# Performance work log

Measured on AMD Instinct MI355X. Metric: run time of the kernel, lower is better.

The kernel has to match this reference:

```python
import jax, jax.numpy as jnp
import numpy as np

XZ = jnp.array([0, 2])
XY = jnp.array([0, 1])
YZ = jnp.array([1, 2])


def _bilinear(plane, uv):
    """plane: (C,R,R) as (C,H,W); uv: (N,2) in [0,1], uv[:,0]->width, uv[:,1]->height.
    Border padding + align_corners=True semantics (grid_sample style)."""
    R = plane.shape[-1]
    xy = jnp.clip(uv, 0.0, 1.0) * (R - 1)
    x, y = xy[:, 0], xy[:, 1]
    x0 = jnp.floor(x)
    y0 = jnp.floor(y)
    x0i = jnp.clip(x0.astype(jnp.int32), 0, R - 1)
    y0i = jnp.clip(y0.astype(jnp.int32), 0, R - 1)
    x1i = jnp.clip(x0i + 1, 0, R - 1)
    y1i = jnp.clip(y0i + 1, 0, R - 1)
    wx = (x - x0)[None, :]  # (1,N)
    wy = (y - y0)[None, :]
    f00 = plane[:, y0i, x0i]  # (C,N)
    f01 = plane[:, y0i, x1i]
    f10 = plane[:, y1i, x0i]
    f11 = plane[:, y1i, x1i]
    top = f00 * (1.0 - wx) + f01 * wx
    bot = f10 * (1.0 - wx) + f11 * wx
    return (top * (1.0 - wy) + bot * wy).T  # (N,C)


def _sample_triplane(p, c_xz, c_xy, c_yz):
    """p: (bs,N,3) in [0,1]; planes: (bs,C,R,R). Returns (bs,N,C) summed over planes."""
    def per_batch(pb, fxz, fxy, fyz):
        return (_bilinear(fxz, pb[:, XZ])
                + _bilinear(fxy, pb[:, XY])
                + _bilinear(fyz, pb[:, YZ]))
    return jax.vmap(per_batch)(p, c_xz, c_xy, c_yz)


def setup_inputs() -> dict:
    key = jax.random.key(0)
    ks = jax.random.split(key, 12)
    bs, ns, C, S, R = 2, 50000, 32, 8, 128
    inp = {
        "query_pos": jax.random.uniform(ks[0], (bs, ns, 3), dtype=jnp.float32),
        "c_xz": jax.random.normal(ks[1], (bs, C, R, R), dtype=jnp.float32),
        "c_xy": jax.random.normal(ks[2], (bs, C, R, R), dtype=jnp.float32),
        "c_yz": jax.random.normal(ks[3], (bs, C, R, R), dtype=jnp.float32),
        # offset weights scaled small so sampled points stay mostly in-bounds
        "W_off": jax.random.normal(ks[4], (C, S * 3), dtype=jnp.float32) * 0.01,
        "b_off": jnp.zeros((S * 3,), dtype=jnp.float32),
        "W_w": jax.random.normal(ks[5], (C, S), dtype=jnp.float32) * 0.1,
        "b_w": jnp.zeros((S,), dtype=jnp.float32),
        "W_v": jax.random.normal(ks[6], (C, C), dtype=jnp.float32) * (1.0 / np.sqrt(C)),
        "b_v": jnp.zeros((C,), dtype=jnp.float32),
        "W_out": jax.random.normal(ks[7], (C, C), dtype=jnp.float32) * (1.0 / np.sqrt(C)),
        "b_out": jnp.zeros((C,), dtype=jnp.float32),
    }
    return inp


def reference(query_pos, c_xz, c_xy, c_yz, W_off, b_off, W_w, b_w, W_v, b_v, W_out, b_out):
    bs, ns, _ = query_pos.shape
    S = W_w.shape[1]
    # round 1: sample tri-plane features at query points
    feature = _sample_triplane(query_pos, c_xz, c_xy, c_yz)  # (bs,ns,C)
    # predict per-query sample offsets and weights
    off = (feature @ W_off + b_off).reshape(bs, ns, S, 3)
    w = (feature @ W_w + b_w).reshape(bs, ns, S, 1)
    pts = off + query_pos[:, :, None, :]  # (bs,ns,S,3)
    # round 2: sample at deformed points
    aux = _sample_triplane(pts.reshape(bs, ns * S, 3), c_xz, c_xy, c_yz)
    v = aux.reshape(bs, ns, S, -1) @ W_v + b_v  # (bs,ns,S,C)
    out = (v * w).sum(-2)                        # weighted reduce over samples
    out = out @ W_out + b_out + feature          # residual
    return out  # (bs,ns,C)
```

## Files before the change

kernel.cpp:

```cpp
#include <hip/hip_runtime.h>
#include <hip/hip_fp16.h>

#define BS 2
#define NS 50000
#define CCH 32
#define RR 128
#define SS 8

typedef float v2f __attribute__((ext_vector_type(2)));
typedef _Float16 h2 __attribute__((ext_vector_type(2)));

#if __has_builtin(__builtin_amdgcn_fdot2)
#define HAVE_DOT2 1
#else
#define HAVE_DOT2 0
#endif


__global__ __launch_bounds__(256)
void prep(const float* __restrict__ cxz,
          const float* __restrict__ cxy,
          const float* __restrict__ cyz,
          const float* __restrict__ Wv, const float* __restrict__ bv,
          const float* __restrict__ Wout,
          unsigned* __restrict__ tp, float* __restrict__ Wc,
          float* __restrict__ bvw) {
    __shared__ float lds[32 * 129];
    int tid = threadIdx.x;
    int row = blockIdx.x;
    if (row < BS * 3 * RR) {
        int y  = row & 127;
        int pl = (row >> 7) % 3;
        int b  = row / 384;
        const float* src = (pl == 0) ? cxz : ((pl == 1) ? cxy : cyz);
        const float* sp = src + (((size_t)(b * CCH)) << 14) + (y << 7);
#pragma unroll
        for (int i = 0; i < 16; ++i) {
            int c = (tid >> 7) + 2 * i;
            int x = tid & 127;
            lds[c * 129 + x] = sp[((size_t)c << 14) + x];
        }
        __syncthreads();
        unsigned* dst = tp + ((size_t)row << 12);
#pragma unroll
        for (int i = 0; i < 16; ++i) {
            int idx = tid + 256 * i;
            int c = idx & 31;
            int x = idx >> 5;
            int x1 = min(x + 1, 127);
            unsigned h0 = __half_as_ushort(__float2half(lds[c * 129 + x]));
            unsigned h1 = __half_as_ushort(__float2half(lds[c * 129 + x1]));
            dst[(x << 5) + c] = h0 | (h1 << 16);
        }
    } else {
        int t = (row - BS * 3 * RR) * 256 + tid;
        int c = t >> 5, j = t & 31;
        float acc = 0.f;
#pragma unroll
        for (int k = 0; k < 32; ++k) acc += Wv[c * 32 + k] * Wout[k * 32 + j];
        Wc[t] = acc;
        if (t < 32) {
            float a2 = 0.f;
#pragma unroll
            for (int k = 0; k < 32; ++k) a2 += bv[k] * Wout[k * 32 + t];
            bvw[t] = a2;
        }
    }
}


struct f4 { v2f lo, hi; };

struct Samp { uint4 u[6]; float wc0, wc1, wr1, wr2; };

__device__ __forceinline__ Samp load_samp(const uint4* __restrict__ P0,
                                          float p0, float p1, float p2) {
    Samp t;
    float x0c = fminf(fmaxf(p0, 0.f), 1.f) * 127.f;
    float x1c = fminf(fmaxf(p1, 0.f), 1.f) * 127.f;
    float x2c = fminf(fmaxf(p2, 0.f), 1.f) * 127.f;
    int i0 = min((int)x0c, 126);
    t.wc0 = x0c - (float)i0;
    int i1 = min((int)x1c, 126);
    t.wc1 = x1c - (float)i1;
    float f1 = floorf(x1c);
    int r10 = (int)f1, r11 = min(r10 + 1, 127);
    t.wr1 = x1c - f1;
    float f2 = floorf(x2c);
    int r20 = (int)f2, r21 = min(r20 + 1, 127);
    t.wr2 = x2c - f2;

    const uint4* Pxz = P0;
    const uint4* Pxy = P0 + (1 << 17);
    const uint4* Pyz = P0 + (2 << 17);
    int c0 = i0 << 3, c1 = i1 << 3;
    int R10 = r10 << 10, R11 = r11 << 10;
    int R20 = r20 << 10, R21 = r21 << 10;
    t.u[0] = Pxz[R20 + c0];  t.u[1] = Pxz[R21 + c0];
    t.u[2] = Pxy[R10 + c0];  t.u[3] = Pxy[R11 + c0];
    t.u[4] = Pyz[R20 + c1];  t.u[5] = Pyz[R21 + c1];
    return t;
}

__device__ __forceinline__ unsigned pack2(float a, float b) {
#if HAVE_DOT2
    return __builtin_bit_cast(unsigned, __builtin_amdgcn_cvt_pkrtz(a, b));
#else
    __half2 h = __floats2half2_rn(a, b);
    return __builtin_bit_cast(unsigned, h);
#endif
}

#if HAVE_DOT2
__device__ __forceinline__ void eval_row(f4& acc, uint4 u, h2 w) {
    acc.lo.x = __builtin_amdgcn_fdot2(__builtin_bit_cast(h2, u.x), w, acc.lo.x, false);
    acc.lo.y = __builtin_amdgcn_fdot2(__builtin_bit_cast(h2, u.y), w, acc.lo.y, false);
    acc.hi.x = __builtin_amdgcn_fdot2(__builtin_bit_cast(h2, u.z), w, acc.hi.x, false);
    acc.hi.y = __builtin_amdgcn_fdot2(__builtin_bit_cast(h2, u.w), w, acc.hi.y, false);
}

__device__ __forceinline__ void eval_plane(f4& acc, uint4 ua, uint4 ub,
                                           float wx, float wy) {
    float wB1 = wx * wy;
    float wB0 = wx - wB1;
    float wA1 = wy - wB1;
    float wA0 = 1.f - wx - wA1;
    h2 w0 = __builtin_bit_cast(h2, __builtin_amdgcn_cvt_pkrtz(wA0, wB0));
    h2 w1 = __builtin_bit_cast(h2, __builtin_amdgcn_cvt_pkrtz(wA1, wB1));
    eval_row(acc, ua, w0);
    eval_row(acc, ub, w1);
}

__device__ __forceinline__ void eval_rowp(f4& acc, uint4 u, unsigned pw) {
    eval_row(acc, u, __builtin_bit_cast(h2, pw));
}
#else
__device__ __forceinline__ void eval_row(f4& acc, uint4 u, float wA, float wB) {
    __half2 h0 = __builtin_bit_cast(__half2, u.x);
    __half2 h1 = __builtin_bit_cast(__half2, u.y);
    __half2 h2_ = __builtin_bit_cast(__half2, u.z);
    __half2 h3 = __builtin_bit_cast(__half2, u.w);
    acc.lo.x = fmaf(__half2float(h0.y), wB, fmaf(__half2float(h0.x), wA, acc.lo.x));
    acc.lo.y = fmaf(__half2float(h1.y), wB, fmaf(__half2float(h1.x), wA, acc.lo.y));
    acc.hi.x = fmaf(__half2float(h2_.y), wB, fmaf(__half2float(h2_.x), wA, acc.hi.x));
    acc.hi.y = fmaf(__half2float(h3.y), wB, fmaf(__half2float(h3.x), wA, acc.hi.y));
}

__device__ __forceinline__ void eval_plane(f4& acc, uint4 ua, uint4 ub,
                                           float wx, float wy) {
    float wB1 = wx * wy;
    float wB0 = wx - wB1;
    float wA1 = wy - wB1;
    float wA0 = 1.f - wx - wA1;
    eval_row(acc, ua, wA0, wB0);
    eval_row(acc, ub, wA1, wB1);
}

__device__ __forceinline__ void eval_rowp(f4& acc, uint4 u, unsigned pw) {
    __half2 hw = __builtin_bit_cast(__half2, pw);
    eval_row(acc, u, __half2float(hw.x), __half2float(hw.y));
}
#endif

__device__ __forceinline__ void eval_samp(const Samp& t, f4& acc) {
    eval_plane(acc, t.u[0], t.u[1], t.wc0, t.wr2);
    eval_plane(acc, t.u[2], t.u[3], t.wc0, t.wr1);
    eval_plane(acc, t.u[4], t.u[5], t.wc1, t.wr2);
}

#define GETE(v, idx) (((idx) & 2) ? (((idx) & 1) ? (v).hi.y : (v).hi.x) \
                                  : (((idx) & 1) ? (v).lo.y : (v).lo.x))
#define GETC(v, idx) __shfl(GETE(v, idx), base | ((idx) >> 2), 64)

struct SampB { uint4 u[6]; };

__global__ __launch_bounds__(256)
void eda_main(const float* __restrict__ qp, const unsigned* __restrict__ tp,
              const float* __restrict__ Woff, const float* __restrict__ boff,
              const float* __restrict__ Ww, const float* __restrict__ bw,
              const float* __restrict__ Wc, const float* __restrict__ bvw,
              const float* __restrict__ bout, float* __restrict__ out) {
    __shared__ float    sWcat[32][32];
    __shared__ unsigned sWc2h[16][32];
    __shared__ float sbcat[32];
    __shared__ float sbvw[32];
    __shared__ float sbout[32];

    int tid = threadIdx.x;
    int lane = tid & 7;
    int base = tid & 56;
    int b  = blockIdx.x & 1;
    int qi = (blockIdx.x >> 1) * 32 + (tid >> 3);
    int qq = min(qi, NS - 1);

    const float* p = qp + ((size_t)b * NS + qq) * 3;
    float p0 = p[0], p1 = p[1], p2 = p[2];

    const uint4* P0 = (const uint4*)tp + (((size_t)(b * 3)) << 17) + lane;

    Samp fs = load_samp(P0, p0, p1, p2);

    for (int i = tid; i < 1024; i += 256) {
        int k = i >> 5, j = i & 31, l2 = j >> 2, e = j & 3;
        sWcat[k][j] = (e < 3) ? Woff[k * 24 + 3 * l2 + e] : Ww[k * 8 + l2];
    }
    {
        int k2 = tid >> 5, j = tid & 31;
        sWc2h[k2][j]     = pack2(Wc[k2 * 64 + j],        Wc[k2 * 64 + 32 + j]);
        sWc2h[k2 + 8][j] = pack2(Wc[(k2 + 8) * 64 + j],  Wc[(k2 + 8) * 64 + 32 + j]);
    }
    if (tid < 32) {
        int l2 = tid >> 2, e = tid & 3;
        sbcat[tid] = (e < 3) ? boff[3 * l2 + e] : bw[l2];
        sbvw[tid]  = bvw[tid];
        sbout[tid] = bout[tid];
    }
    __syncthreads();

    f4 feat; feat.lo = (v2f){0.f, 0.f}; feat.hi = (v2f){0.f, 0.f};
    eval_samp(fs, feat);

    f4 cat;
    cat.lo.x = sbcat[(lane << 2) + 0]; cat.lo.y = sbcat[(lane << 2) + 1];
    cat.hi.x = sbcat[(lane << 2) + 2]; cat.hi.y = sbcat[(lane << 2) + 3];
#pragma unroll
    for (int k = 0; k < 32; ++k) {
        float fc = GETC(feat, k);
        const v2f* wp = (const v2f*)&sWcat[k][lane << 2];
        v2f fc2 = {fc, fc};
        cat.lo = __builtin_elementwise_fma(fc2, wp[0], cat.lo);
        cat.hi = __builtin_elementwise_fma(fc2, wp[1], cat.hi);
    }

    float sx = p0 + cat.lo.x, sy = p1 + cat.lo.y, sz = p2 + cat.hi.x;
    float wt_my = cat.hi.y;
    float x0c = fminf(fmaxf(sx, 0.f), 1.f) * 127.f;
    int  i0 = min((int)x0c, 126);
    float wc0 = x0c - (float)i0;
    float x1c = fminf(fmaxf(sy, 0.f), 1.f) * 127.f;
    int  i1 = min((int)x1c, 126);
    float wc1 = x1c - (float)i1;
    float f1 = floorf(x1c);
    int r10 = (int)f1, r11 = min(r10 + 1, 127);
    float wr1 = x1c - f1;
    float x2c = fminf(fmaxf(sz, 0.f), 1.f) * 127.f;
    float f2 = floorf(x2c);
    int r20 = (int)f2, r21 = min(r20 + 1, 127);
    float wr2 = x2c - f2;
    int c0 = i0 << 3, c1 = i1 << 3;
    int o0 = (r20 << 10) + c0;
    int o1 = (r21 << 10) + c0;
    int o2 = (1 << 17) + (r10 << 10) + c0;
    int o3 = (1 << 17) + (r11 << 10) + c0;
    int o4 = (2 << 17) + (r20 << 10) + c1;
    int o5 = (2 << 17) + (r21 << 10) + c1;
    unsigned m0, m1, m2, m3, m4, m5;
    { float wB1 = wc0 * wr2, wB0 = wc0 - wB1, wA1 = wr2 - wB1, wA0 = 1.f - wc0 - wA1;
      m0 = pack2(wA0, wB0); m1 = pack2(wA1, wB1); }
    { float wB1 = wc0 * wr1, wB0 = wc0 - wB1, wA1 = wr1 - wB1, wA0 = 1.f - wc0 - wA1;
      m2 = pack2(wA0, wB0); m3 = pack2(wA1, wB1); }
    { float wB1 = wc1 * wr2, wB0 = wc1 - wB1, wA1 = wr2 - wB1, wA0 = 1.f - wc1 - wA1;
      m4 = pack2(wA0, wB0); m5 = pack2(wA1, wB1); }

    f4 wa; wa.lo = (v2f){0.f, 0.f}; wa.hi = (v2f){0.f, 0.f};
    float wsum = 0.f;
    SampB cur, nxt;
    {
        int src = base;
        cur.u[0] = P0[__shfl(o0, src, 64)];
        cur.u[1] = P0[__shfl(o1, src, 64)];
        cur.u[2] = P0[__shfl(o2, src, 64)];
        cur.u[3] = P0[__shfl(o3, src, 64)];
        cur.u[4] = P0[__shfl(o4, src, 64)];
        cur.u[5] = P0[__shfl(o5, src, 64)];
    }
#pragma unroll
    for (int s = 0; s < SS; ++s) {
        if (s < SS - 1) {
            int src = base | (s + 1);
            nxt.u[0] = P0[__shfl(o0, src, 64)];
            nxt.u[1] = P0[__shfl(o1, src, 64)];
            nxt.u[2] = P0[__shfl(o2, src, 64)];
            nxt.u[3] = P0[__shfl(o3, src, 64)];
            nxt.u[4] = P0[__shfl(o4, src, 64)];
            nxt.u[5] = P0[__shfl(o5, src, 64)];
        }
        int src = base | s;
        f4 aux; aux.lo = (v2f){0.f, 0.f}; aux.hi = (v2f){0.f, 0.f};
        eval_rowp(aux, cur.u[0], (unsigned)__shfl((int)m0, src, 64));
        eval_rowp(aux, cur.u[1], (unsigned)__shfl((int)m1, src, 64));
        eval_rowp(aux, cur.u[2], (unsigned)__shfl((int)m2, src, 64));
        eval_rowp(aux, cur.u[3], (unsigned)__shfl((int)m3, src, 64));
        eval_rowp(aux, cur.u[4], (unsigned)__shfl((int)m4, src, 64));
        eval_rowp(aux, cur.u[5], (unsigned)__shfl((int)m5, src, 64));
        float wt = __shfl(wt_my, src, 64);
        v2f w2 = {wt, wt};
        wa.lo = __builtin_elementwise_fma(w2, aux.lo, wa.lo);
        wa.hi = __builtin_elementwise_fma(w2, aux.hi, wa.hi);
        wsum += wt;
        if (s < SS - 1) cur = nxt;
    }

    f4 o;
    v2f ws2 = {wsum, wsum};
    {
        v2f bo  = {sbout[(lane << 2) + 0], sbout[(lane << 2) + 1]};
        v2f bv2 = {sbvw[(lane << 2) + 0], sbvw[(lane << 2) + 1]};
        o.lo = __builtin_elementwise_fma(ws2, bv2, bo) + feat.lo;
        v2f bo2 = {sbout[(lane << 2) + 2], sbout[(lane << 2) + 3]};
        v2f bv3 = {sbvw[(lane << 2) + 2], sbvw[(lane << 2) + 3]};
        o.hi = __builtin_elementwise_fma(ws2, bv3, bo2) + feat.hi;
    }
    unsigned pkLo = pack2(wa.lo.x, wa.lo.y);
    unsigned pkHi = pack2(wa.hi.x, wa.hi.y);
#pragma unroll
    for (int k2 = 0; k2 < 16; ++k2) {
        unsigned wb = (unsigned)__shfl((int)((k2 & 1) ? pkHi : pkLo), base | (k2 >> 1), 64);
        const uint4 wv = *(const uint4*)&sWc2h[k2][lane << 2];
#if HAVE_DOT2
        h2 wp = __builtin_bit_cast(h2, wb);
        o.lo.x = __builtin_amdgcn_fdot2(__builtin_bit_cast(h2, wv.x), wp, o.lo.x, false);
        o.lo.y = __builtin_amdgcn_fdot2(__builtin_bit_cast(h2, wv.y), wp, o.lo.y, false);
        o.hi.x = __builtin_amdgcn_fdot2(__builtin_bit_cast(h2, wv.z), wp, o.hi.x, false);
        o.hi.y = __builtin_amdgcn_fdot2(__builtin_bit_cast(h2, wv.w), wp, o.hi.y, false);
#else
        __half2 hw = __builtin_bit_cast(__half2, wb);
        float a0 = __half2float(hw.x), a1 = __half2float(hw.y);
        __half2 w0 = __builtin_bit_cast(__half2, wv.x);
        __half2 w1 = __builtin_bit_cast(__half2, wv.y);
        __half2 w2_ = __builtin_bit_cast(__half2, wv.z);
        __half2 w3 = __builtin_bit_cast(__half2, wv.w);
        o.lo.x = fmaf(__half2float(w0.y), a1, fmaf(__half2float(w0.x), a0, o.lo.x));
        o.lo.y = fmaf(__half2float(w1.y), a1, fmaf(__half2float(w1.x), a0, o.lo.y));
        o.hi.x = fmaf(__half2float(w2_.y), a1, fmaf(__half2float(w2_.x), a0, o.hi.x));
        o.hi.y = fmaf(__half2float(w3.y), a1, fmaf(__half2float(w3.x), a0, o.hi.y));
#endif
    }

    if (qi < NS) {
        float* dst = out + ((size_t)b * NS + qi) * 32 + (lane << 2);
        *(float4*)dst = make_float4(o.lo.x, o.lo.y, o.hi.x, o.hi.y);
    }
}

extern "C" void kernel_launch(void* const* d_in, const int* in_sizes, int n_in,
                              void* d_out, int out_size, void* d_ws, size_t ws_size,
                              hipStream_t stream) {
    const float* qp   = (const float*)d_in[0];
    const float* cxz  = (const float*)d_in[1];
    const float* cxy  = (const float*)d_in[2];
    const float* cyz  = (const float*)d_in[3];
    const float* Woff = (const float*)d_in[4];
    const float* boff = (const float*)d_in[5];
    const float* Ww   = (const float*)d_in[6];
    const float* bw   = (const float*)d_in[7];
    const float* Wv   = (const float*)d_in[8];
    const float* bv   = (const float*)d_in[9];
    const float* Wout = (const float*)d_in[10];
    const float* bout = (const float*)d_in[11];
    float* out = (float*)d_out;

    unsigned* tp = (unsigned*)d_ws;
    float* Wc  = (float*)((char*)d_ws + (size_t)BS * 3 * RR * RR * CCH * 4);
    float* bvw = Wc + 1024;

    prep<<<BS * 3 * RR + 4, 256, 0, stream>>>(cxz, cxy, cyz, Wv, bv, Wout, tp, Wc, bvw);
    int blocks_per_batch = (NS + 31) / 32;
    eda_main<<<2 * blocks_per_batch, 256, 0, stream>>>(qp, tp, Woff, boff, Ww, bw,
                                                       Wc, bvw, bout, out);
}
```

Measured before the change: 129.4 us.

## Store triplane as plain fp16 texels instead of x-pair packed layout

The prep kernel now writes each plane texel once as fp16, with channels contiguous and vectorized float4 reads and uint4 writes. Before, each texel was stored next to its x+1 neighbour in a packed pair. This halves the workspace and the prep write traffic. In exchange the main kernel issues twice as many gathers (two uint2 loads per corner row instead of one uint4) and drops the fdot2 path for scalar half-to-float FMAs. Interpolation weights are also shuffled as packed half fractions, which lowers their precision.

```diff
diff --git a/kernel.cpp b/kernel.cpp
--- a/kernel.cpp
+++ b/kernel.cpp
@@ -16,6 +16,12 @@
 #define HAVE_DOT2 0
 #endif
 
+
+__device__ __forceinline__ unsigned pk_rn(float a, float b) {
+    unsigned h0 = __half_as_ushort(__float2half(a));
+    unsigned h1 = __half_as_ushort(__float2half(b));
+    return h0 | (h1 << 16);
+}
 
 __global__ __launch_bounds__(256)
 void prep(const float* __restrict__ cxz,
@@ -34,23 +40,30 @@
         int b  = row / 384;
         const float* src = (pl == 0) ? cxz : ((pl == 1) ? cxy : cyz);
         const float* sp = src + (((size_t)(b * CCH)) << 14) + (y << 7);
-#pragma unroll
-        for (int i = 0; i < 16; ++i) {
-            int c = (tid >> 7) + 2 * i;
-            int x = tid & 127;
-            lds[c * 129 + x] = sp[((size_t)c << 14) + x];
+        int c = tid >> 3, xq = tid & 7;
+        const float4* s4 = (const float4*)(sp + ((size_t)c << 14));
+#pragma unroll
+        for (int k = 0; k < 4; ++k) {
+            float4 v = s4[xq + 8 * k];
+            int x = (xq + 8 * k) << 2;
+            lds[c * 129 + x + 0] = v.x;
+            lds[c * 129 + x + 1] = v.y;
+            lds[c * 129 + x + 2] = v.z;
+            lds[c * 129 + x + 3] = v.w;
         }
         __syncthreads();
-        unsigned* dst = tp + ((size_t)row << 12);
-#pragma unroll
-        for (int i = 0; i < 16; ++i) {
-            int idx = tid + 256 * i;
-            int c = idx & 31;
-            int x = idx >> 5;
-            int x1 = min(x + 1, 127);
-            unsigned h0 = __half_as_ushort(__float2half(lds[c * 129 + x]));
-            unsigned h1 = __half_as_ushort(__float2half(lds[c * 129 + x1]));
-            dst[(x << 5) + c] = h0 | (h1 << 16);
+        uint4* dst = (uint4*)(tp + ((size_t)row << 11));
+#pragma unroll
+        for (int t = 0; t < 2; ++t) {
+            int j = tid + 256 * t;
+            int x  = j >> 2;
+            int cb = (j & 3) << 3;
+            uint4 o;
+            o.x = pk_rn(lds[(cb + 0) * 129 + x], lds[(cb + 1) * 129 + x]);
+            o.y = pk_rn(lds[(cb + 2) * 129 + x], lds[(cb + 3) * 129 + x]);
+            o.z = pk_rn(lds[(cb + 4) * 129 + x], lds[(cb + 5) * 129 + x]);
+            o.w = pk_rn(lds[(cb + 6) * 129 + x], lds[(cb + 7) * 129 + x]);
+            dst[j] = o;
         }
     } else {
         int t = (row - BS * 3 * RR) * 256 + tid;
@@ -71,35 +84,71 @@
 
 struct f4 { v2f lo, hi; };
 
-struct Samp { uint4 u[6]; float wc0, wc1, wr1, wr2; };
-
-__device__ __forceinline__ Samp load_samp(const uint4* __restrict__ P0,
-                                          float p0, float p1, float p2) {
-    Samp t;
+struct Coord {
+    int o0, o1, o2, o3, o4, o5;
+    float wc0, wc1, wr1, wr2;
+};
+
+__device__ __forceinline__ Coord coord(float p0, float p1, float p2) {
+    Coord c;
     float x0c = fminf(fmaxf(p0, 0.f), 1.f) * 127.f;
+    int i0 = min((int)x0c, 126);
+    c.wc0 = x0c - (float)i0;
     float x1c = fminf(fmaxf(p1, 0.f), 1.f) * 127.f;
-    float x2c = fminf(fmaxf(p2, 0.f), 1.f) * 127.f;
-    int i0 = min((int)x0c, 126);
-    t.wc0 = x0c - (float)i0;
     int i1 = min((int)x1c, 126);
-    t.wc1 = x1c - (float)i1;
+    c.wc1 = x1c - (float)i1;
     float f1 = floorf(x1c);
     int r10 = (int)f1, r11 = min(r10 + 1, 127);
-    t.wr1 = x1c - f1;
+    c.wr1 = x1c - f1;
+    float x2c = fminf(fmaxf(p2, 0.f), 1.f) * 127.f;
     float f2 = floorf(x2c);
     int r20 = (int)f2, r21 = min(r20 + 1, 127);
-    t.wr2 = x2c - f2;
-
-    const uint4* Pxz = P0;
-    const uint4* Pxy = P0 + (1 << 17);
-    const uint4* Pyz = P0 + (2 << 17);
+    c.wr2 = x2c - f2;
     int c0 = i0 << 3, c1 = i1 << 3;
-    int R10 = r10 << 10, R11 = r11 << 10;
-    int R20 = r20 << 10, R21 = r21 << 10;
-    t.u[0] = Pxz[R20 + c0];  t.u[1] = Pxz[R21 + c0];
-    t.u[2] = Pxy[R10 + c0];  t.u[3] = Pxy[R11 + c0];
-    t.u[4] = Pyz[R20 + c1];  t.u[5] = Pyz[R21 + c1];
-    return t;
+    c.o0 = (r20 << 10) + c0;
+    c.o1 = (r21 << 10) + c0;
+    c.o2 = (1 << 17) + (r10 << 10) + c0;
+    c.o3 = (1 << 17) + (r11 << 10) + c0;
+    c.o4 = (2 << 17) + (r20 << 10) + c1;
+    c.o5 = (2 << 17) + (r21 << 10) + c1;
+    return c;
+}
+
+struct Samp12 { uint2 u[12]; };
+
+__device__ __forceinline__ void load6x2(const uint2* __restrict__ P0, Samp12& t,
+                                        int o0, int o1, int o2, int o3, int o4, int o5) {
+    t.u[0]  = P0[o0]; t.u[1]  = P0[o0 + 8];
+    t.u[2]  = P0[o1]; t.u[3]  = P0[o1 + 8];
+    t.u[4]  = P0[o2]; t.u[5]  = P0[o2 + 8];
+    t.u[6]  = P0[o3]; t.u[7]  = P0[o3 + 8];
+    t.u[8]  = P0[o4]; t.u[9]  = P0[o4 + 8];
+    t.u[10] = P0[o5]; t.u[11] = P0[o5 + 8];
+}
+
+__device__ __forceinline__ void eval_col(f4& a, uint2 u, float w) {
+    __half2 h0 = __builtin_bit_cast(__half2, u.x);
+    __half2 h1 = __builtin_bit_cast(__half2, u.y);
+    a.lo.x = fmaf(__half2float(h0.x), w, a.lo.x);
+    a.lo.y = fmaf(__half2float(h0.y), w, a.lo.y);
+    a.hi.x = fmaf(__half2float(h1.x), w, a.hi.x);
+    a.hi.y = fmaf(__half2float(h1.y), w, a.hi.y);
+}
+
+__device__ __forceinline__ void eval_plane2(f4& a, const uint2* u, float wx, float wy) {
+    float wB1 = wx * wy;
+    float wB0 = wx - wB1;
+    float wA1 = wy - wB1;
+    float wA0 = 1.f - wx - wA1;
+    eval_col(a, u[0], wA0); eval_col(a, u[1], wB0);
+    eval_col(a, u[2], wA1); eval_col(a, u[3], wB1);
+}
+
+__device__ __forceinline__ void eval12(const Samp12& t, f4& a,
+                                       float wc0, float wc1, float wr1, float wr2) {
+    eval_plane2(a, t.u + 0, wc0, wr2);
+    eval_plane2(a, t.u + 4, wc0, wr1);
+    eval_plane2(a, t.u + 8, wc1, wr2);
 }
 
 __device__ __forceinline__ unsigned pack2(float a, float b) {
@@ -111,68 +160,9 @@
 #endif
 }
 
-#if HAVE_DOT2
-__device__ __forceinline__ void eval_row(f4& acc, uint4 u, h2 w) {
-    acc.lo.x = __builtin_amdgcn_fdot2(__builtin_bit_cast(h2, u.x), w, acc.lo.x, false);
-    acc.lo.y = __builtin_amdgcn_fdot2(__builtin_bit_cast(h2, u.y), w, acc.lo.y, false);
-    acc.hi.x = __builtin_amdgcn_fdot2(__builtin_bit_cast(h2, u.z), w, acc.hi.x, false);
-    acc.hi.y = __builtin_amdgcn_fdot2(__builtin_bit_cast(h2, u.w), w, acc.hi.y, false);
-}
-
-__device__ __forceinline__ void eval_plane(f4& acc, uint4 ua, uint4 ub,
-                                           float wx, float wy) {
-    float wB1 = wx * wy;
-    float wB0 = wx - wB1;
-    float wA1 = wy - wB1;
-    float wA0 = 1.f - wx - wA1;
-    h2 w0 = __builtin_bit_cast(h2, __builtin_amdgcn_cvt_pkrtz(wA0, wB0));
-    h2 w1 = __builtin_bit_cast(h2, __builtin_amdgcn_cvt_pkrtz(wA1, wB1));
-    eval_row(acc, ua, w0);
-    eval_row(acc, ub, w1);
-}
-
-__device__ __forceinline__ void eval_rowp(f4& acc, uint4 u, unsigned pw) {
-    eval_row(acc, u, __builtin_bit_cast(h2, pw));
-}
-#else
-__device__ __forceinline__ void eval_row(f4& acc, uint4 u, float wA, float wB) {
-    __half2 h0 = __builtin_bit_cast(__half2, u.x);
-    __half2 h1 = __builtin_bit_cast(__half2, u.y);
-    __half2 h2_ = __builtin_bit_cast(__half2, u.z);
-    __half2 h3 = __builtin_bit_cast(__half2, u.w);
-    acc.lo.x = fmaf(__half2float(h0.y), wB, fmaf(__half2float(h0.x), wA, acc.lo.x));
-    acc.lo.y = fmaf(__half2float(h1.y), wB, fmaf(__half2float(h1.x), wA, acc.lo.y));
-    acc.hi.x = fmaf(__half2float(h2_.y), wB, fmaf(__half2float(h2_.x), wA, acc.hi.x));
-    acc.hi.y = fmaf(__half2float(h3.y), wB, fmaf(__half2float(h3.x), wA, acc.hi.y));
-}
-
-__device__ __forceinline__ void eval_plane(f4& acc, uint4 ua, uint4 ub,
-                                           float wx, float wy) {
-    float wB1 = wx * wy;
-    float wB0 = wx - wB1;
-    float wA1 = wy - wB1;
-    float wA0 = 1.f - wx - wA1;
-    eval_row(acc, ua, wA0, wB0);
-    eval_row(acc, ub, wA1, wB1);
-}
-
-__device__ __forceinline__ void eval_rowp(f4& acc, uint4 u, unsigned pw) {
-    __half2 hw = __builtin_bit_cast(__half2, pw);
-    eval_row(acc, u, __half2float(hw.x), __half2float(hw.y));
-}
-#endif
-
-__device__ __forceinline__ void eval_samp(const Samp& t, f4& acc) {
-    eval_plane(acc, t.u[0], t.u[1], t.wc0, t.wr2);
-    eval_plane(acc, t.u[2], t.u[3], t.wc0, t.wr1);
-    eval_plane(acc, t.u[4], t.u[5], t.wc1, t.wr2);
-}
-
 #define GETE(v, idx) (((idx) & 2) ? (((idx) & 1) ? (v).hi.y : (v).hi.x) \
                                   : (((idx) & 1) ? (v).lo.y : (v).lo.x))
 #define GETC(v, idx) __shfl(GETE(v, idx), base | ((idx) >> 2), 64)
-
-struct SampB { uint4 u[6]; };
 
 __global__ __launch_bounds__(256)
 void eda_main(const float* __restrict__ qp, const unsigned* __restrict__ tp,
@@ -196,9 +186,11 @@
     const float* p = qp + ((size_t)b * NS + qq) * 3;
     float p0 = p[0], p1 = p[1], p2 = p[2];
 
-    const uint4* P0 = (const uint4*)tp + (((size_t)(b * 3)) << 17) + lane;
-
-    Samp fs = load_samp(P0, p0, p1, p2);
+    const uint2* P0 = (const uint2*)tp + (((size_t)(b * 3)) << 17) + lane;
+
+    Coord fc = coord(p0, p1, p2);
+    Samp12 fs;
+    load6x2(P0, fs, fc.o0, fc.o1, fc.o2, fc.o3, fc.o4, fc.o5);
 
     for (int i = tid; i < 1024; i += 256) {
         int k = i >> 5, j = i & 31, l2 = j >> 2, e = j & 3;
@@ -218,81 +210,49 @@
     __syncthreads();
 
     f4 feat; feat.lo = (v2f){0.f, 0.f}; feat.hi = (v2f){0.f, 0.f};
-    eval_samp(fs, feat);
+    eval12(fs, feat, fc.wc0, fc.wc1, fc.wr1, fc.wr2);
 
     f4 cat;
     cat.lo.x = sbcat[(lane << 2) + 0]; cat.lo.y = sbcat[(lane << 2) + 1];
     cat.hi.x = sbcat[(lane << 2) + 2]; cat.hi.y = sbcat[(lane << 2) + 3];
 #pragma unroll
     for (int k = 0; k < 32; ++k) {
-        float fc = GETC(feat, k);
+        float fcv = GETC(feat, k);
         const v2f* wp = (const v2f*)&sWcat[k][lane << 2];
-        v2f fc2 = {fc, fc};
+        v2f fc2 = {fcv, fcv};
         cat.lo = __builtin_elementwise_fma(fc2, wp[0], cat.lo);
         cat.hi = __builtin_elementwise_fma(fc2, wp[1], cat.hi);
     }
 
-    float sx = p0 + cat.lo.x, sy = p1 + cat.lo.y, sz = p2 + cat.hi.x;
+    Coord my = coord(p0 + cat.lo.x, p1 + cat.lo.y, p2 + cat.hi.x);
     float wt_my = cat.hi.y;
-    float x0c = fminf(fmaxf(sx, 0.f), 1.f) * 127.f;
-    int  i0 = min((int)x0c, 126);
-    float wc0 = x0c - (float)i0;
-    float x1c = fminf(fmaxf(sy, 0.f), 1.f) * 127.f;
-    int  i1 = min((int)x1c, 126);
-    float wc1 = x1c - (float)i1;
-    float f1 = floorf(x1c);
-    int r10 = (int)f1, r11 = min(r10 + 1, 127);
-    float wr1 = x1c - f1;
-    float x2c = fminf(fmaxf(sz, 0.f), 1.f) * 127.f;
-    float f2 = floorf(x2c);
-    int r20 = (int)f2, r21 = min(r20 + 1, 127);
-    float wr2 = x2c - f2;
-    int c0 = i0 << 3, c1 = i1 << 3;
-    int o0 = (r20 << 10) + c0;
-    int o1 = (r21 << 10) + c0;
-    int o2 = (1 << 17) + (r10 << 10) + c0;
-    int o3 = (1 << 17) + (r11 << 10) + c0;
-    int o4 = (2 << 17) + (r20 << 10) + c1;
-    int o5 = (2 << 17) + (r21 << 10) + c1;
-    unsigned m0, m1, m2, m3, m4, m5;
-    { float wB1 = wc0 * wr2, wB0 = wc0 - wB1, wA1 = wr2 - wB1, wA0 = 1.f - wc0 - wA1;
-      m0 = pack2(wA0, wB0); m1 = pack2(wA1, wB1); }
-    { float wB1 = wc0 * wr1, wB0 = wc0 - wB1, wA1 = wr1 - wB1, wA0 = 1.f - wc0 - wA1;
-      m2 = pack2(wA0, wB0); m3 = pack2(wA1, wB1); }
-    { float wB1 = wc1 * wr2, wB0 = wc1 - wB1, wA1 = wr2 - wB1, wA0 = 1.f - wc1 - wA1;
-      m4 = pack2(wA0, wB0); m5 = pack2(wA1, wB1); }
+    unsigned pf01 = pack2(my.wc0, my.wc1);
+    unsigned pf23 = pack2(my.wr1, my.wr2);
 
     f4 wa; wa.lo = (v2f){0.f, 0.f}; wa.hi = (v2f){0.f, 0.f};
     float wsum = 0.f;
-    SampB cur, nxt;
+    Samp12 cur, nxt;
     {
         int src = base;
-        cur.u[0] = P0[__shfl(o0, src, 64)];
-        cur.u[1] = P0[__shfl(o1, src, 64)];
-        cur.u[2] = P0[__shfl(o2, src, 64)];
-        cur.u[3] = P0[__shfl(o3, src, 64)];
-        cur.u[4] = P0[__shfl(o4, src, 64)];
-        cur.u[5] = P0[__shfl(o5, src, 64)];
+        load6x2(P0, cur, __shfl(my.o0, src, 64), __shfl(my.o1, src, 64),
+                         __shfl(my.o2, src, 64), __shfl(my.o3, src, 64),
+                         __shfl(my.o4, src, 64), __shfl(my.o5, src, 64));
     }
 #pragma unroll
     for (int s = 0; s < SS; ++s) {
         if (s < SS - 1) {
             int src = base | (s + 1);
-            nxt.u[0] = P0[__shfl(o0, src, 64)];
-            nxt.u[1] = P0[__shfl(o1, src, 64)];
-            nxt.u[2] = P0[__shfl(o2, src, 64)];
-            nxt.u[3] = P0[__shfl(o3, src, 64)];
-            nxt.u[4] = P0[__shfl(o4, src, 64)];
-            nxt.u[5] = P0[__shfl(o5, src, 64)];
+            load6x2(P0, nxt, __shfl(my.o0, src, 64), __shfl(my.o1, src, 64),
+                             __shfl(my.o2, src, 64), __shfl(my.o3, src, 64),
+                             __shfl(my.o4, src, 64), __shfl(my.o5, src, 64));
         }
         int src = base | s;
+        __half2 f01 = __builtin_bit_cast(__half2, (unsigned)__shfl((int)pf01, src, 64));
+        __half2 f23 = __builtin_bit_cast(__half2, (unsigned)__shfl((int)pf23, src, 64));
+        float wc0 = __half2float(f01.x), wc1 = __half2float(f01.y);
+        float wr1 = __half2float(f23.x), wr2 = __half2float(f23.y);
         f4 aux; aux.lo = (v2f){0.f, 0.f}; aux.hi = (v2f){0.f, 0.f};
-        eval_rowp(aux, cur.u[0], (unsigned)__shfl((int)m0, src, 64));
-        eval_rowp(aux, cur.u[1], (unsigned)__shfl((int)m1, src, 64));
-        eval_rowp(aux, cur.u[2], (unsigned)__shfl((int)m2, src, 64));
-        eval_rowp(aux, cur.u[3], (unsigned)__shfl((int)m3, src, 64));
-        eval_rowp(aux, cur.u[4], (unsigned)__shfl((int)m4, src, 64));
-        eval_rowp(aux, cur.u[5], (unsigned)__shfl((int)m5, src, 64));
+        eval12(cur, aux, wc0, wc1, wr1, wr2);
         float wt = __shfl(wt_my, src, 64);
         v2f w2 = {wt, wt};
         wa.lo = __builtin_elementwise_fma(w2, aux.lo, wa.lo);
@@ -361,7 +321,7 @@
     float* out = (float*)d_out;
 
     unsigned* tp = (unsigned*)d_ws;
-    float* Wc  = (float*)((char*)d_ws + (size_t)BS * 3 * RR * RR * CCH * 4);
+    float* Wc  = (float*)((char*)d_ws + (size_t)BS * 3 * RR * RR * CCH * 2);
     float* bvw = Wc + 1024;
 
     prep<<<BS * 3 * RR + 4, 256, 0, stream>>>(cxz, cxy, cyz, Wv, bv, Wout, tp, Wc, bvw);
```

Result: slower. 137.7 us (+6.4%).

## Deepen gather prefetch to two samples and fold sample weights into bilinear weights

Applied to the files above, without the earlier changes.

The main kernel now prefetches gathered triplane texels two samples ahead instead of one, so more memory loads are in flight per lane. Each sample's attention weight is pre-multiplied into its packed fp16 bilinear weights and accumulated straight into the output, which removes the per-sample aux accumulator, the weight shuffle and the FMA. The weight sum is now a butterfly reduction. The prep kernel reads float4 vectors and writes uint4 packed outputs to widen memory transactions. This costs more registers and may lower occupancy, and multiplying the weights before fp16 packing changes rounding slightly.

```diff
diff --git a/kernel.cpp b/kernel.cpp
--- a/kernel.cpp
+++ b/kernel.cpp
@@ -16,6 +16,12 @@
 #define HAVE_DOT2 0
 #endif
 
+
+__device__ __forceinline__ unsigned pk_rn(float a, float b) {
+    unsigned h0 = __half_as_ushort(__float2half(a));
+    unsigned h1 = __half_as_ushort(__float2half(b));
+    return h0 | (h1 << 16);
+}
 
 __global__ __launch_bounds__(256)
 void prep(const float* __restrict__ cxz,
@@ -34,23 +40,31 @@
         int b  = row / 384;
         const float* src = (pl == 0) ? cxz : ((pl == 1) ? cxy : cyz);
         const float* sp = src + (((size_t)(b * CCH)) << 14) + (y << 7);
-#pragma unroll
-        for (int i = 0; i < 16; ++i) {
-            int c = (tid >> 7) + 2 * i;
-            int x = tid & 127;
-            lds[c * 129 + x] = sp[((size_t)c << 14) + x];
+        int c = tid >> 3, xq = tid & 7;
+        const float4* s4 = (const float4*)(sp + ((size_t)c << 14));
+#pragma unroll
+        for (int k = 0; k < 4; ++k) {
+            float4 v = s4[xq + 8 * k];
+            int x = (xq + 8 * k) << 2;
+            lds[c * 129 + x + 0] = v.x;
+            lds[c * 129 + x + 1] = v.y;
+            lds[c * 129 + x + 2] = v.z;
+            lds[c * 129 + x + 3] = v.w;
         }
         __syncthreads();
-        unsigned* dst = tp + ((size_t)row << 12);
-#pragma unroll
-        for (int i = 0; i < 16; ++i) {
-            int idx = tid + 256 * i;
-            int c = idx & 31;
-            int x = idx >> 5;
+        uint4* dst = (uint4*)(tp + ((size_t)row << 12));
+#pragma unroll
+        for (int i = 0; i < 4; ++i) {
+            int j = tid + 256 * i;
+            int x  = j >> 3;
+            int c0 = (j & 7) << 2;
             int x1 = min(x + 1, 127);
-            unsigned h0 = __half_as_ushort(__float2half(lds[c * 129 + x]));
-            unsigned h1 = __half_as_ushort(__float2half(lds[c * 129 + x1]));
-            dst[(x << 5) + c] = h0 | (h1 << 16);
+            uint4 o;
+            o.x = pk_rn(lds[(c0 + 0) * 129 + x], lds[(c0 + 0) * 129 + x1]);
+            o.y = pk_rn(lds[(c0 + 1) * 129 + x], lds[(c0 + 1) * 129 + x1]);
+            o.z = pk_rn(lds[(c0 + 2) * 129 + x], lds[(c0 + 2) * 129 + x1]);
+            o.w = pk_rn(lds[(c0 + 3) * 129 + x], lds[(c0 + 3) * 129 + x1]);
+            dst[j] = o;
         }
     } else {
         int t = (row - BS * 3 * RR) * 256 + tid;
@@ -72,6 +86,7 @@
 struct f4 { v2f lo, hi; };
 
 struct Samp { uint4 u[6]; float wc0, wc1, wr1, wr2; };
+struct SampB { uint4 u[6]; };
 
 __device__ __forceinline__ Samp load_samp(const uint4* __restrict__ P0,
                                           float p0, float p1, float p2) {
@@ -172,8 +187,6 @@
                                   : (((idx) & 1) ? (v).lo.y : (v).lo.x))
 #define GETC(v, idx) __shfl(GETE(v, idx), base | ((idx) >> 2), 64)
 
-struct SampB { uint4 u[6]; };
-
 __global__ __launch_bounds__(256)
 void eda_main(const float* __restrict__ qp, const unsigned* __restrict__ tp,
               const float* __restrict__ Woff, const float* __restrict__ boff,
@@ -225,9 +238,9 @@
     cat.hi.x = sbcat[(lane << 2) + 2]; cat.hi.y = sbcat[(lane << 2) + 3];
 #pragma unroll
     for (int k = 0; k < 32; ++k) {
-        float fc = GETC(feat, k);
+        float fcv = GETC(feat, k);
         const v2f* wp = (const v2f*)&sWcat[k][lane << 2];
-        v2f fc2 = {fc, fc};
+        v2f fc2 = {fcv, fcv};
         cat.lo = __builtin_elementwise_fma(fc2, wp[0], cat.lo);
         cat.hi = __builtin_elementwise_fma(fc2, wp[1], cat.hi);
     }
@@ -256,49 +269,51 @@
     int o5 = (2 << 17) + (r21 << 10) + c1;
     unsigned m0, m1, m2, m3, m4, m5;
     { float wB1 = wc0 * wr2, wB0 = wc0 - wB1, wA1 = wr2 - wB1, wA0 = 1.f - wc0 - wA1;
-      m0 = pack2(wA0, wB0); m1 = pack2(wA1, wB1); }
+      m0 = pack2(wA0 * wt_my, wB0 * wt_my); m1 = pack2(wA1 * wt_my, wB1 * wt_my); }
     { float wB1 = wc0 * wr1, wB0 = wc0 - wB1, wA1 = wr1 - wB1, wA0 = 1.f - wc0 - wA1;
-      m2 = pack2(wA0, wB0); m3 = pack2(wA1, wB1); }
+      m2 = pack2(wA0 * wt_my, wB0 * wt_my); m3 = pack2(wA1 * wt_my, wB1 * wt_my); }
     { float wB1 = wc1 * wr2, wB0 = wc1 - wB1, wA1 = wr2 - wB1, wA0 = 1.f - wc1 - wA1;
-      m4 = pack2(wA0, wB0); m5 = pack2(wA1, wB1); }
+      m4 = pack2(wA0 * wt_my, wB0 * wt_my); m5 = pack2(wA1 * wt_my, wB1 * wt_my); }
+
+    float wsum = wt_my;
+    wsum += __shfl_xor(wsum, 1, 64);
+    wsum += __shfl_xor(wsum, 2, 64);
+    wsum += __shfl_xor(wsum, 4, 64);
 
     f4 wa; wa.lo = (v2f){0.f, 0.f}; wa.hi = (v2f){0.f, 0.f};
-    float wsum = 0.f;
-    SampB cur, nxt;
+    SampB sA, sB;
     {
         int src = base;
-        cur.u[0] = P0[__shfl(o0, src, 64)];
-        cur.u[1] = P0[__shfl(o1, src, 64)];
-        cur.u[2] = P0[__shfl(o2, src, 64)];
-        cur.u[3] = P0[__shfl(o3, src, 64)];
-        cur.u[4] = P0[__shfl(o4, src, 64)];
-        cur.u[5] = P0[__shfl(o5, src, 64)];
+        sA.u[0] = P0[__shfl(o0, src, 64)]; sA.u[1] = P0[__shfl(o1, src, 64)];
+        sA.u[2] = P0[__shfl(o2, src, 64)]; sA.u[3] = P0[__shfl(o3, src, 64)];
+        sA.u[4] = P0[__shfl(o4, src, 64)]; sA.u[5] = P0[__shfl(o5, src, 64)];
+    }
+    {
+        int src = base | 1;
+        sB.u[0] = P0[__shfl(o0, src, 64)]; sB.u[1] = P0[__shfl(o1, src, 64)];
+        sB.u[2] = P0[__shfl(o2, src, 64)]; sB.u[3] = P0[__shfl(o3, src, 64)];
+        sB.u[4] = P0[__shfl(o4, src, 64)]; sB.u[5] = P0[__shfl(o5, src, 64)];
     }
 #pragma unroll
     for (int s = 0; s < SS; ++s) {
-        if (s < SS - 1) {
-            int src = base | (s + 1);
-            nxt.u[0] = P0[__shfl(o0, src, 64)];
-            nxt.u[1] = P0[__shfl(o1, src, 64)];
-            nxt.u[2] = P0[__shfl(o2, src, 64)];
-            nxt.u[3] = P0[__shfl(o3, src, 64)];
-            nxt.u[4] = P0[__shfl(o4, src, 64)];
-            nxt.u[5] = P0[__shfl(o5, src, 64)];
+        SampB sC;
+        if (s + 2 < SS) {
+            int src = base | (s + 2);
+            sC.u[0] = P0[__shfl(o0, src, 64)]; sC.u[1] = P0[__shfl(o1, src, 64)];
+            sC.u[2] = P0[__shfl(o2, src, 64)]; sC.u[3] = P0[__shfl(o3, src, 64)];
+            sC.u[4] = P0[__shfl(o4, src, 64)]; sC.u[5] = P0[__shfl(o5, src, 64)];
         }
         int src = base | s;
-        f4 aux; aux.lo = (v2f){0.f, 0.f}; aux.hi = (v2f){0.f, 0.f};
-        eval_rowp(aux, cur.u[0], (unsigned)__shfl((int)m0, src, 64));
-        eval_rowp(aux, cur.u[1], (unsigned)__shfl((int)m1, src, 64));
-        eval_rowp(aux, cur.u[2], (unsigned)__shfl((int)m2, src, 64));
-        eval_rowp(aux, cur.u[3], (unsigned)__shfl((int)m3, src, 64));
-        eval_rowp(aux, cur.u[4], (unsigned)__shfl((int)m4, src, 64));
-        eval_rowp(aux, cur.u[5], (unsigned)__shfl((int)m5, src, 64));
-        float wt = __shfl(wt_my, src, 64);
-        v2f w2 = {wt, wt};
-        wa.lo = __builtin_elementwise_fma(w2, aux.lo, wa.lo);
-        wa.hi = __builtin_elementwise_fma(w2, aux.hi, wa.hi);
-        wsum += wt;
-        if (s < SS - 1) cur = nxt;
+        eval_rowp(wa, sA.u[0], (unsigned)__shfl((int)m0, src, 64));
+        eval_rowp(wa, sA.u[1], (unsigned)__shfl((int)m1, src, 64));
+        eval_rowp(wa, sA.u[2], (unsigned)__shfl((int)m2, src, 64));
+        eval_rowp(wa, sA.u[3], (unsigned)__shfl((int)m3, src, 64));
+        eval_rowp(wa, sA.u[4], (unsigned)__shfl((int)m4, src, 64));
+        eval_rowp(wa, sA.u[5], (unsigned)__shfl((int)m5, src, 64));
+        if (s + 1 < SS) {
+            sA = sB;
+            if (s + 2 < SS) sB = sC;
+        }
     }
 
     f4 o;
```

Measured after the change: 132.2 us. 1.02x slower.
